# Kernel tuning notes

Measured on AMD Instinct MI355X. Metric: run time of the kernel, lower is better.

The kernel has to match this reference:

```python
import jax, jax.numpy as jnp
import numpy as np

B, C_IN, C_BOT, H = 256, 48, 8, 4096
SCALE = 1.0 / np.sqrt(8.0).astype(np.float32)


def setup_inputs() -> dict:
    key = jax.random.key(0)
    k1, k2, k3 = jax.random.split(key, 3)
    x = jax.random.normal(k1, (B, C_IN, H, 1), dtype=jnp.float32)
    # 1x1 conv weights, stored as [out_channels, in_channels]
    w_down = jax.random.normal(k2, (C_BOT, C_IN), dtype=jnp.float32) * (1.0 / np.sqrt(C_IN))
    w_up = jax.random.normal(k3, (C_IN, C_BOT), dtype=jnp.float32) * (1.0 / np.sqrt(C_BOT))
    return {"x": x, "w_down": w_down, "w_up": w_up}


def reference(x, w_down, w_up):
    # x: [B, 48, H, 1] -> [B, 48, H]
    xs = jnp.squeeze(x, axis=3)
    # fc_down applied (identically) for k, q, v: same weights, same input
    kqv = jnp.einsum('oc,bch->boh', w_down, xs)  # [B, 8, H]
    # attention matrix over channel dim: [B, 8, 8]
    am = jax.nn.softmax(jnp.einsum('bih,bjh->bij', kqv, kqv) * SCALE, axis=-1)
    z = jnp.einsum('bij,bjh->bih', am, kqv)       # [B, 8, H]
    out = jnp.einsum('co,boh->bch', w_up, z)      # [B, 48, H]
    return out[..., None]                          # [B, 48, H, 1]
```

## Files before the change

kernel.cpp:

```cpp
#include <hip/hip_runtime.h>

#define B_    256
#define CIN   48
#define CBOT  8
#define H_    4096
#define SCALE_ 0.35355339059327373f

#define NT    512
#define HHALF 2048

__global__ __launch_bounds__(NT, 4) void ultimus_half(
    const float* __restrict__ x,
    const float* __restrict__ w_down,
    const float* __restrict__ w_up,
    float* __restrict__ out)
{
    const int s = blockIdx.x;
    const int b = blockIdx.y;
    const int t = threadIdx.x;

    __shared__ float s_wdT[CIN * CBOT];
    __shared__ float s_red[8 * 36];
    __shared__ float s_am [CBOT * CBOT];
    __shared__ float s_M  [CIN * CBOT];

    if (t < CIN * CBOT) {
        const int c = t >> 3, o = t & 7;
        s_wdT[t] = w_down[o * CIN + c];
    }
    __syncthreads();

    const float* xb = x + (size_t)b * (CIN * H_);
    const int hO = s * HHALF + (t << 2);
    const int hT = (1 - s) * HHALF + (t << 2);

    float accO[CBOT][4], accT[CBOT][4];
    #pragma unroll
    for (int o = 0; o < CBOT; ++o) {
        accO[o][0] = accO[o][1] = accO[o][2] = accO[o][3] = 0.0f;
        accT[o][0] = accT[o][1] = accT[o][2] = accT[o][3] = 0.0f;
    }

    #pragma unroll 4
    for (int c = 0; c < CIN; ++c) {
        const float4 xvO = *reinterpret_cast<const float4*>(xb + (size_t)c * H_ + hO);
        const float4 xvT = *reinterpret_cast<const float4*>(xb + (size_t)c * H_ + hT);
        #pragma unroll
        for (int o = 0; o < CBOT; ++o) {
            const float w = s_wdT[c * CBOT + o];
            accO[o][0] += w * xvO.x;  accO[o][1] += w * xvO.y;
            accO[o][2] += w * xvO.z;  accO[o][3] += w * xvO.w;
            accT[o][0] += w * xvT.x;  accT[o][1] += w * xvT.y;
            accT[o][2] += w * xvT.z;  accT[o][3] += w * xvT.w;
        }
    }

    float g[36];
    {
        int idx = 0;
        #pragma unroll
        for (int i = 0; i < CBOT; ++i) {
            #pragma unroll
            for (int j = i; j < CBOT; ++j, ++idx) {
                g[idx] = accO[i][0] * accO[j][0] + accO[i][1] * accO[j][1]
                       + accO[i][2] * accO[j][2] + accO[i][3] * accO[j][3]
                       + accT[i][0] * accT[j][0] + accT[i][1] * accT[j][1]
                       + accT[i][2] * accT[j][2] + accT[i][3] * accT[j][3];
            }
        }
    }
    #pragma unroll
    for (int k = 0; k < 36; ++k) {
        float v = g[k];
        v += __shfl_down(v, 32, 64);
        v += __shfl_down(v, 16, 64);
        v += __shfl_down(v,  8, 64);
        v += __shfl_down(v,  4, 64);
        v += __shfl_down(v,  2, 64);
        v += __shfl_down(v,  1, 64);
        g[k] = v;
    }
    const int wave = t >> 6;
    const int lane = t & 63;
    if (lane == 0) {
        #pragma unroll
        for (int k = 0; k < 36; ++k) s_red[wave * 36 + k] = g[k];
    }
    __syncthreads();
    if (t < 36) {
        float v = 0.0f;
        #pragma unroll
        for (int w = 0; w < 8; ++w) v += s_red[w * 36 + t];
        s_red[t] = v;
    }
    __syncthreads();

    if (t < 8) {
        float row[8];
        #pragma unroll
        for (int j = 0; j < 8; ++j) {
            const int i2 = t < j ? t : j;
            const int j2 = t < j ? j : t;
            const int tri = i2 * 8 - (i2 * (i2 - 1)) / 2 + (j2 - i2);
            row[j] = s_red[tri] * SCALE_;
        }
        float m = row[0];
        #pragma unroll
        for (int j = 1; j < 8; ++j) m = fmaxf(m, row[j]);
        float sum = 0.0f;
        #pragma unroll
        for (int j = 0; j < 8; ++j) { row[j] = __expf(row[j] - m); sum += row[j]; }
        const float inv = 1.0f / sum;
        #pragma unroll
        for (int j = 0; j < 8; ++j) s_am[t * 8 + j] = row[j] * inv;
    }
    __syncthreads();

    if (t < CIN * CBOT) {
        const int c = t >> 3, j = t & 7;
        float v = 0.0f;
        #pragma unroll
        for (int o = 0; o < CBOT; ++o)
            v += w_up[c * CBOT + o] * s_am[o * CBOT + j];
        s_M[t] = v;
    }
    __syncthreads();

    float* ob = out + (size_t)b * (CIN * H_) + hO;
    #pragma unroll 8
    for (int c = 0; c < CIN; ++c) {
        float4 r;
        r.x = r.y = r.z = r.w = 0.0f;
        #pragma unroll
        for (int j = 0; j < CBOT; ++j) {
            const float mcj = s_M[c * CBOT + j];
            r.x += mcj * accO[j][0];
            r.y += mcj * accO[j][1];
            r.z += mcj * accO[j][2];
            r.w += mcj * accO[j][3];
        }
        *reinterpret_cast<float4*>(ob + (size_t)c * H_) = r;
    }
}

extern "C" void kernel_launch(void* const* d_in, const int* in_sizes, int n_in,
                              void* d_out, int out_size, void* d_ws, size_t ws_size,
                              hipStream_t stream) {
    const float* x      = (const float*)d_in[0];
    const float* w_down = (const float*)d_in[1];
    const float* w_up   = (const float*)d_in[2];
    float* out          = (float*)d_out;

    hipLaunchKernelGGL(ultimus_half, dim3(2, B_), dim3(NT), 0, stream,
                       x, w_down, w_up, out);
}
```

Measured before the change: 380.6 us.

## Use 1024-thread blocks covering full H with half-row writes and nontemporal stores

Result: slower. 399.4 us (+4.9%).

```diff
diff --git a/kernel.cpp b/kernel.cpp
--- a/kernel.cpp
+++ b/kernel.cpp
@@ -6,21 +6,23 @@
 #define H_    4096
 #define SCALE_ 0.35355339059327373f
 
-#define NT    512
-#define HHALF 2048
 
-__global__ __launch_bounds__(NT, 4) void ultimus_half(
+typedef float vf4 __attribute__((ext_vector_type(4)));
+
+__global__ __launch_bounds__(1024, 8) void ultimus_tlp(
     const float* __restrict__ x,
     const float* __restrict__ w_down,
     const float* __restrict__ w_up,
     float* __restrict__ out)
 {
-    const int s = blockIdx.x;
-    const int b = blockIdx.y;
-    const int t = threadIdx.x;
+    const int L  = blockIdx.x;
+    const int jj = L & 15;
+    const int b  = ((L >> 4) << 3) | (jj & 7);
+    const int s  = jj >> 3;
+    const int t  = threadIdx.x;
 
     __shared__ float s_wdT[CIN * CBOT];
-    __shared__ float s_red[8 * 36];
+    __shared__ float s_red[16 * 36];
     __shared__ float s_am [CBOT * CBOT];
     __shared__ float s_M  [CIN * CBOT];
 
@@ -30,28 +32,24 @@
     }
     __syncthreads();
 
-    const float* xb = x + (size_t)b * (CIN * H_);
-    const int hO = s * HHALF + (t << 2);
-    const int hT = (1 - s) * HHALF + (t << 2);
+    const int h0 = t << 2;
+    const float* xb = x + (size_t)b * (CIN * H_) + h0;
 
-    float accO[CBOT][4], accT[CBOT][4];
+    float acc[CBOT][4];
     #pragma unroll
-    for (int o = 0; o < CBOT; ++o) {
-        accO[o][0] = accO[o][1] = accO[o][2] = accO[o][3] = 0.0f;
-        accT[o][0] = accT[o][1] = accT[o][2] = accT[o][3] = 0.0f;
-    }
+    for (int o = 0; o < CBOT; ++o)
+        acc[o][0] = acc[o][1] = acc[o][2] = acc[o][3] = 0.0f;
 
-    #pragma unroll 4
+    #pragma unroll 8
     for (int c = 0; c < CIN; ++c) {
-        const float4 xvO = *reinterpret_cast<const float4*>(xb + (size_t)c * H_ + hO);
-        const float4 xvT = *reinterpret_cast<const float4*>(xb + (size_t)c * H_ + hT);
+        const vf4 xv = *reinterpret_cast<const vf4*>(xb + (size_t)c * H_);
         #pragma unroll
         for (int o = 0; o < CBOT; ++o) {
             const float w = s_wdT[c * CBOT + o];
-            accO[o][0] += w * xvO.x;  accO[o][1] += w * xvO.y;
-            accO[o][2] += w * xvO.z;  accO[o][3] += w * xvO.w;
-            accT[o][0] += w * xvT.x;  accT[o][1] += w * xvT.y;
-            accT[o][2] += w * xvT.z;  accT[o][3] += w * xvT.w;
+            acc[o][0] += w * xv.x;
+            acc[o][1] += w * xv.y;
+            acc[o][2] += w * xv.z;
+            acc[o][3] += w * xv.w;
         }
     }
 
@@ -62,10 +60,8 @@
         for (int i = 0; i < CBOT; ++i) {
             #pragma unroll
             for (int j = i; j < CBOT; ++j, ++idx) {
-                g[idx] = accO[i][0] * accO[j][0] + accO[i][1] * accO[j][1]
-                       + accO[i][2] * accO[j][2] + accO[i][3] * accO[j][3]
-                       + accT[i][0] * accT[j][0] + accT[i][1] * accT[j][1]
-                       + accT[i][2] * accT[j][2] + accT[i][3] * accT[j][3];
+                g[idx] = acc[i][0] * acc[j][0] + acc[i][1] * acc[j][1]
+                       + acc[i][2] * acc[j][2] + acc[i][3] * acc[j][3];
             }
         }
     }
@@ -87,10 +83,11 @@
         for (int k = 0; k < 36; ++k) s_red[wave * 36 + k] = g[k];
     }
     __syncthreads();
+
     if (t < 36) {
         float v = 0.0f;
         #pragma unroll
-        for (int w = 0; w < 8; ++w) v += s_red[w * 36 + t];
+        for (int w = 0; w < 16; ++w) v += s_red[w * 36 + t];
         s_red[t] = v;
     }
     __syncthreads();
@@ -126,20 +123,22 @@
     }
     __syncthreads();
 
-    float* ob = out + (size_t)b * (CIN * H_) + hO;
-    #pragma unroll 8
-    for (int c = 0; c < CIN; ++c) {
-        float4 r;
-        r.x = r.y = r.z = r.w = 0.0f;
-        #pragma unroll
-        for (int j = 0; j < CBOT; ++j) {
-            const float mcj = s_M[c * CBOT + j];
-            r.x += mcj * accO[j][0];
-            r.y += mcj * accO[j][1];
-            r.z += mcj * accO[j][2];
-            r.w += mcj * accO[j][3];
+    if ((t >> 9) == s) {
+        float* ob = out + (size_t)b * (CIN * H_) + h0;
+        #pragma unroll 8
+        for (int c = 0; c < CIN; ++c) {
+            vf4 r;
+            r.x = r.y = r.z = r.w = 0.0f;
+            #pragma unroll
+            for (int j = 0; j < CBOT; ++j) {
+                const float mcj = s_M[c * CBOT + j];
+                r.x += mcj * acc[j][0];
+                r.y += mcj * acc[j][1];
+                r.z += mcj * acc[j][2];
+                r.w += mcj * acc[j][3];
+            }
+            __builtin_nontemporal_store(r, reinterpret_cast<vf4*>(ob + (size_t)c * H_));
         }
-        *reinterpret_cast<float4*>(ob + (size_t)c * H_) = r;
     }
 }
 
@@ -151,6 +150,6 @@
     const float* w_up   = (const float*)d_in[2];
     float* out          = (float*)d_out;
 
-    hipLaunchKernelGGL(ultimus_half, dim3(2, B_), dim3(NT), 0, stream,
+    hipLaunchKernelGGL(ultimus_tlp, dim3(2 * B_), dim3(1024), 0, stream,
                        x, w_down, w_up, out);
 }
```
